# Kernel optimization log

Hardware: AMD Instinct MI355X
Metric: run time of the kernel (lower is better)

Reference implementation:

```python
import jax, jax.numpy as jnp
import numpy as np

UNITS = 64
NUM_LEVELS = 4
ORDER = 4  # order=-1 defaults to num_levels
NUM_FEATURES = 64  # 63 input features + 1 time channel
LEN_TENSORS = NUM_LEVELS * (NUM_LEVELS + 1) // 2  # 10


def setup_inputs() -> dict:
    key = jax.random.key(0)
    k1, k2 = jax.random.split(key)
    X = jax.random.normal(k1, (32, 2048, 63), dtype=jnp.float32)
    # learned low-rank kernel [num_features, len_tensors, units]; small scale keeps
    # higher-level signature products numerically tame
    kernel = jax.random.normal(k2, (NUM_FEATURES, LEN_TENSORS, UNITS), dtype=jnp.float32) * 0.02
    return {"X": X, "kernel": kernel}


def _ecumsum(x):
    # exclusive cumulative sum along time axis (axis=1), forward direction
    return jnp.cumsum(x, axis=1) - x


def reference(X, kernel):
    B, T, _ = X.shape
    # add_time=True: linear time channel in [-1, 1]
    t = jnp.arange(T, dtype=X.dtype) * (2.0 / (T - 1.0)) - 1.0
    time = jnp.broadcast_to(t[None, :, None], (B, T, 1))
    Xa = jnp.concatenate([time, X], axis=-1)  # [B, T, F]
    # low-rank projection: [B, T, len_tensors, units]
    M = jnp.einsum('btf,fku->btku', Xa, kernel)
    # difference=True: forward increments, zero-padded at t=0
    M = jnp.concatenate([jnp.zeros_like(M[:, :1]), M[:, 1:] - M[:, :-1]], axis=1)

    # level 1
    out = jnp.sum(M[..., 0, :], axis=1)  # [B, units]

    k = 1
    for m in range(1, NUM_LEVELS):
        R = [M[..., k, :]]  # list of [B, T, units]
        k += 1
        for i in range(1, m + 1):
            d = min(i + 1, ORDER)
            A = sum(R)
            Mk = M[..., k, :]
            R_next = [Mk * _ecumsum(A)]
            for j in range(1, d):
                R_next.append(Mk * R[j - 1] / jnp.asarray(j + 1, dtype=X.dtype))
            k += 1
            R = R_next
        out = out + jnp.sum(sum(R), axis=1)
    return out
```

## Files before the change

kernel.cpp:

```cpp
#include <hip/hip_runtime.h>


#define TT 2048
#define NFX 63
#define KT 10
#define NU 64
#define NQS 18
#define NCC 32
#define NSEG 4

#define MAPS_BYTES (32u * NCC * NQS * NU * 4u)
#define PLANE      40960u

typedef __attribute__((ext_vector_type(16))) float f32x16v;
typedef __attribute__((ext_vector_type(8)))  short bf16x8v;


__device__ __forceinline__ unsigned short bf16_rne(float x) {
  unsigned int u = __float_as_uint(x);
  unsigned int r = (u + 0x7FFFu + ((u >> 16) & 1u)) >> 16;
  return (unsigned short)r;
}
__device__ __forceinline__ float bf16f(unsigned short h) {
  return __uint_as_float(((unsigned int)h) << 16);
}

__device__ __forceinline__ void compose_ab(const float* q1, const float* q2,
                                           float* r)
{
  r[0] = q1[0] + q2[0] + q2[1]*q1[4] + q2[2]*q1[5] + q2[3]*q1[6];
  r[1] = q1[1] + q2[1];
  r[2] = q1[2] + q2[2] + q1[7]*q2[3];
  r[3] = q1[3] + q2[3];
  r[4] = q1[4] + q2[4];
  r[5] = q1[5] + q2[5];
  r[6] = q1[6] + q2[6] + q2[7]*q1[5];
  r[7] = q1[7] + q2[7];
}

__device__ __forceinline__ void compose_c(const float* q1, const float* q2,
                                          float* r)
{
  r[0] = q1[0] + q2[0] + q2[1]*q1[4] + q2[2]*q1[5] + q2[3]*q1[6];
  r[1] = q1[1] + q2[1] + q1[7]*q2[2] + q1[9]*q2[3];
  r[2] = q1[2] + q2[2] + q1[8]*q2[3];
  r[3] = q1[3] + q2[3];
  r[4] = q1[4] + q2[4];
  r[5] = q1[5] + q2[5] + q2[7]*q1[4];
  r[6] = q1[6] + q2[6] + q2[8]*q1[5] + q2[9]*q1[4];
  r[7] = q1[7] + q2[7];
  r[8] = q1[8] + q2[8];
  r[9] = q1[9] + q2[9] + q2[8]*q1[7];
}

__global__ __launch_bounds__(256)
void lrsig_prep_kernel(const float* __restrict__ Kw,
                       unsigned short* __restrict__ kwb)
{
  int e = blockIdx.x * 256 + threadIdx.x;
  int j  = e & 7;
  int l  = (e >> 3) & 63;
  int ks = (e >> 9) & 3;
  int ub = (e >> 11) & 1;
  int nt = e >> 12;
  int f = ks * 16 + (l >> 5) * 8 + j;
  int u = ub * 32 + (l & 31);
  float x = Kw[(f * KT + nt) * NU + u];
  unsigned short hi = bf16_rne(x);
  unsigned short lo = bf16_rne(x - bf16f(hi));
  kwb[e] = hi;
  kwb[PLANE + e] = lo;
}

#define LOADB(S) do {                                                        \
  _Pragma("unroll")                                                          \
  for (int ks = 0; ks < 4; ++ks) {                                           \
    const unsigned short* bp = kwb + ((((S) * 2 + ub) * 4 + ks) * 512) + l*8;\
    bh[ks] = *(const bf16x8v*)(bp);                                          \
    bl[ks] = *(const bf16x8v*)(bp + PLANE);                                  \
  } } while (0)

#define MFMA12(ACC) do {                                                     \
  _Pragma("unroll")                                                          \
  for (int ks = 0; ks < 4; ++ks) {                                           \
    ACC = __builtin_amdgcn_mfma_f32_32x32x16_bf16(ah[ks], bh[ks], ACC, 0,0,0); \
    ACC = __builtin_amdgcn_mfma_f32_32x32x16_bf16(al[ks], bh[ks], ACC, 0,0,0); \
    ACC = __builtin_amdgcn_mfma_f32_32x32x16_bf16(ah[ks], bl[ks], ACC, 0,0,0); \
  } } while (0)

#define ZERO(ACC) do { _Pragma("unroll")                                     \
  for (int zi = 0; zi < 16; ++zi) ACC[zi] = 0.f; } while (0)

__global__ __launch_bounds__(512)
void lrsig_chunk_kernel(const float* __restrict__ X,
                        const unsigned short* __restrict__ kwb,
                        float* __restrict__ wmaps)
{
  __shared__ __align__(16) float smemf[8192];
  char* smem = (char*)smemf;
  float* rawf = smemf + 4096;

  const int b   = blockIdx.y;
  const int c   = blockIdx.x;
  const int tid = threadIdx.x;
  const int l   = tid & 63;
  const int w   = tid >> 6;
  const int cg  = w & 1;
  const int ub  = (w >> 1) & 1;
  const int rt  = w >> 2;
  const int col = l & 31;
  const int hi8 = l >> 5;
  const int t0  = c * 64;

  float sv[8];
  {
    const float* Xb = X + (size_t)b * TT * NFX;
    const int base = (t0 - 1) * NFX;
#pragma unroll
    for (int ii = 0; ii < 8; ++ii) {
      int i = tid + ii * 512;
      int off = base + i + ((c == 0 && i < NFX) ? NFX : 0);
      sv[ii] = (i < 65 * NFX) ? Xb[off] : 0.f;
    }
  }

  bf16x8v bh[4], bl[4];
  LOADB(cg ? 6 : 0);

#pragma unroll
  for (int ii = 0; ii < 8; ++ii) {
    int i = tid + ii * 512;
    if (i < 65 * NFX) rawf[i] = sv[ii];
  }
  __syncthreads();

  {
    float v0[8], v1[8];
#pragma unroll
    for (int ii = 0; ii < 8; ++ii) {
      int e = tid + ii * 512;
      if (e < 64 * NFX) { v0[ii] = rawf[e]; v1[ii] = rawf[e + NFX]; }
    }
#pragma unroll
    for (int ii = 0; ii < 8; ++ii) {
      int e = tid + ii * 512;
      if (e < 64 * NFX) {
        int r2 = e / NFX;
        int c2 = e - r2 * NFX;
        float d = v1[ii] - v0[ii];
        unsigned short h  = bf16_rne(d);
        unsigned short lo = bf16_rne(d - bf16f(h));
        int byte = r2 * 128 + ((2 * (c2 + 1)) ^ ((r2 & 7) << 4));
        *(unsigned short*)(smem + byte)        = h;
        *(unsigned short*)(smem + 8192 + byte) = lo;
      }
    }
  }
  if (tid < 64) {
    int r2 = tid;
    float d = (t0 + r2 == 0) ? 0.f : (2.0f / 2047.0f);
    unsigned short h  = bf16_rne(d);
    unsigned short lo = bf16_rne(d - bf16f(h));
    int byte = r2 * 128 + ((0) ^ ((r2 & 7) << 4));
    *(unsigned short*)(smem + byte)        = h;
    *(unsigned short*)(smem + 8192 + byte) = lo;
  }
  __syncthreads();

  const int row = rt * 32 + col;
  const int colbase = ub * 32 + col;

  bf16x8v ah[4], al[4];
#pragma unroll
  for (int ks = 0; ks < 4; ++ks) {
    const int f0 = ks * 16 + hi8 * 8;
    const int abyte = row * 128 + ((2 * f0) ^ ((row & 7) << 4));
    ah[ks] = *(const bf16x8v*)(smem + abyte);
    al[ks] = *(const bf16x8v*)(smem + 8192 + abyte);
  }

  if (cg == 0) {
    f32x16v acc[6];
    ZERO(acc[0]); ZERO(acc[1]); ZERO(acc[2]);
    ZERO(acc[3]); ZERO(acc[4]); ZERO(acc[5]);
    MFMA12(acc[0]); LOADB(1);
    MFMA12(acc[1]); LOADB(2);
    MFMA12(acc[2]); LOADB(3);
    MFMA12(acc[3]); LOADB(4);
    MFMA12(acc[4]); LOADB(5);
    MFMA12(acc[5]);

    float tot[8];
#pragma unroll
    for (int j = 0; j < 4; ++j) {
      float oA = 0.f, a1 = 0.f, lc1 = 0.f;
      float oB = 0.f, a3 = 0.f, aA = 0.f, lc3 = 0.f, lcA = 0.f, g4 = 0.f;
#pragma unroll
      for (int i = 0; i < 4; ++i) {
        const int r = 4 * j + i;
        float m0 = acc[0][r], m1 = acc[1][r], m2 = acc[2][r];
        float m3 = acc[3][r], m4 = acc[4][r], m5 = acc[5][r];
        oA  += m0 + m2 * (lc1 + 0.5f * m1);
        a1  += m2;
        lc1 += m1;
        float s0 = m4 * lc3;
        float s1 = 0.5f * m4 * m3;
        oB  += m5 * (lcA + 0.5f * s0 + (1.f/3.f) * s1);
        a3  += m5 * (g4 + 0.5f * m4);
        aA  += m5;
        lcA += s0 + s1;
        g4  += m4;
        lc3 += m3;
      }
      float pm[8] = {oA + oB, a1, a3, aA, lc1, lc3, lcA, g4};
      float q1v[8], q2v[8], m8r[8];
#pragma unroll
      for (int q = 0; q < 8; ++q) {
        float oth = __shfl_xor(pm[q], 32);
        q1v[q] = hi8 ? oth : pm[q];
        q2v[q] = hi8 ? pm[q] : oth;
      }
      compose_ab(q1v, q2v, m8r);
      if (j == 0) {
#pragma unroll
        for (int q = 0; q < 8; ++q) tot[q] = m8r[q];
      } else {
        float nx[8];
        compose_ab(tot, m8r, nx);
#pragma unroll
        for (int q = 0; q < 8; ++q) tot[q] = nx[q];
      }
    }
    if (hi8 == 0) {
      float* p = &rawf[(rt * NQS) * NU + colbase];
#pragma unroll
      for (int q = 0; q < 8; ++q) p[q * NU] = tot[q];
    }
  } else {
    f32x16v acc[4];
    ZERO(acc[0]); ZERO(acc[1]); ZERO(acc[2]); ZERO(acc[3]);
    MFMA12(acc[0]); LOADB(7);
    MFMA12(acc[1]); LOADB(8);
    MFMA12(acc[2]); LOADB(9);
    MFMA12(acc[3]);

    float tot[10];
#pragma unroll
    for (int j = 0; j < 4; ++j) {
      float o = 0.f, a6 = 0.f, aP = 0.f, aQ = 0.f;
      float lc6 = 0.f, lcP = 0.f, lcQ = 0.f, g7 = 0.f, g8 = 0.f, hh = 0.f;
#pragma unroll
      for (int i = 0; i < 4; ++i) {
        const int r = 4 * j + i;
        float m6 = acc[0][r], m7 = acc[1][r], m8 = acc[2][r], m9 = acc[3][r];
        float p0 = m7 * lc6;
        float p1 = 0.5f * m7 * m6;
        float q0 = m8 * lcP;
        float q1 = 0.5f * m8 * p0;
        float q2 = (1.f/3.f) * m8 * p1;
        o   += m9 * (lcQ + 0.5f * q0 + (1.f/3.f) * q1 + 0.25f * q2);
        a6  += m9 * (hh + m8 * (0.5f * g7 + (1.f/6.f) * m7));
        aP  += m9 * (g8 + 0.5f * m8);
        aQ  += m9;
        hh  += m8 * (g7 + 0.5f * m7);
        lcP += p0 + p1;
        lcQ += q0 + q1 + q2;
        g7 += m7; g8 += m8; lc6 += m6;
      }
      float pm[10] = {o, a6, aP, aQ, lc6, lcP, lcQ, g7, g8, hh};
      float q1v[10], q2v[10], m8r[10];
#pragma unroll
      for (int q = 0; q < 10; ++q) {
        float oth = __shfl_xor(pm[q], 32);
        q1v[q] = hi8 ? oth : pm[q];
        q2v[q] = hi8 ? pm[q] : oth;
      }
      compose_c(q1v, q2v, m8r);
      if (j == 0) {
#pragma unroll
        for (int q = 0; q < 10; ++q) tot[q] = m8r[q];
      } else {
        float nx[10];
        compose_c(tot, m8r, nx);
#pragma unroll
        for (int q = 0; q < 10; ++q) tot[q] = nx[q];
      }
    }
    if (hi8 == 0) {
      float* p = &rawf[(rt * NQS + 8) * NU + colbase];
#pragma unroll
      for (int q = 0; q < 10; ++q) p[q * NU] = tot[q];
    }
  }
  __syncthreads();

  if (tid < NU) {
    const int uu = tid;
    float q1v[8], q2v[8], rv[8];
#pragma unroll
    for (int q = 0; q < 8; ++q) {
      q1v[q] = rawf[(0 * NQS + q) * NU + uu];
      q2v[q] = rawf[(1 * NQS + q) * NU + uu];
    }
    compose_ab(q1v, q2v, rv);
    float* p = &wmaps[(((size_t)b * NCC + c) * NQS) * NU + uu];
#pragma unroll
    for (int q = 0; q < 8; ++q) p[q * NU] = rv[q];
  } else if (tid < 2 * NU) {
    const int uu = tid - NU;
    float q1v[10], q2v[10], rv[10];
#pragma unroll
    for (int q = 0; q < 10; ++q) {
      q1v[q] = rawf[(0 * NQS + 8 + q) * NU + uu];
      q2v[q] = rawf[(1 * NQS + 8 + q) * NU + uu];
    }
    compose_c(q1v, q2v, rv);
    float* p = &wmaps[(((size_t)b * NCC + c) * NQS + 8) * NU + uu];
#pragma unroll
    for (int q = 0; q < 10; ++q) p[q * NU] = rv[q];
  }
}

__global__ __launch_bounds__(256)
void lrsig_combine_kernel(const float* __restrict__ wmaps,
                          float* __restrict__ out)
{
  __shared__ float sm[NSEG * NQS * NU];
  const int b   = blockIdx.x;
  const int seg = threadIdx.x >> 6;
  const int u   = threadIdx.x & 63;

  float tab[8], tc[10];
  {
    const float* p0 = &wmaps[(((size_t)b * NCC + seg * 8) * NQS) * NU + u];
#pragma unroll
    for (int q = 0; q < 8; ++q)  tab[q] = p0[q * NU];
#pragma unroll
    for (int q = 0; q < 10; ++q) tc[q]  = p0[(8 + q) * NU];
  }
  for (int i = 1; i < 8; ++i) {
    const float* p = &wmaps[(((size_t)b * NCC + seg * 8 + i) * NQS) * NU + u];
    float mab[8], mc[10], rab[8], rc[10];
#pragma unroll
    for (int q = 0; q < 8; ++q)  mab[q] = p[q * NU];
#pragma unroll
    for (int q = 0; q < 10; ++q) mc[q]  = p[(8 + q) * NU];
    compose_ab(tab, mab, rab);
    compose_c(tc, mc, rc);
#pragma unroll
    for (int q = 0; q < 8; ++q)  tab[q] = rab[q];
#pragma unroll
    for (int q = 0; q < 10; ++q) tc[q]  = rc[q];
  }
#pragma unroll
  for (int q = 0; q < 8; ++q)  sm[(seg * NQS + q) * NU + u]     = tab[q];
#pragma unroll
  for (int q = 0; q < 10; ++q) sm[(seg * NQS + 8 + q) * NU + u] = tc[q];
  __syncthreads();

  if (threadIdx.x < NU) {
    const int uu = threadIdx.x;
    float c1 = 0.f, c3 = 0.f, cA = 0.f, c6 = 0.f, cP = 0.f, cQ = 0.f, o = 0.f;
#pragma unroll
    for (int s = 0; s < NSEG; ++s) {
      float q[NQS];
#pragma unroll
      for (int i = 0; i < NQS; ++i) q[i] = sm[(s * NQS + i) * NU + uu];
      o  += q[0] + q[8] + q[1]*c1 + q[2]*c3 + q[3]*cA
          + q[9]*c6 + q[10]*cP + q[11]*cQ;
      cA += q[7]*c3 + q[6];
      cQ += q[16]*cP + q[17]*c6 + q[14];
      cP += q[15]*c6 + q[13];
      c1 += q[4]; c3 += q[5]; c6 += q[12];
    }
    out[b * 64 + uu] = o;
  }
}

extern "C" void kernel_launch(void* const* d_in, const int* in_sizes, int n_in,
                              void* d_out, int out_size, void* d_ws, size_t ws_size,
                              hipStream_t stream) {
  const float* X  = (const float*)d_in[0];
  const float* Kw = (const float*)d_in[1];
  float* out = (float*)d_out;
  float* wmaps = (float*)d_ws;
  unsigned short* kwb = (unsigned short*)((char*)d_ws + MAPS_BYTES);

  hipLaunchKernelGGL(lrsig_prep_kernel, dim3(160), dim3(256), 0, stream,
                     Kw, kwb);
  hipLaunchKernelGGL(lrsig_chunk_kernel, dim3(NCC, 32), dim3(512), 0, stream,
                     X, kwb, wmaps);
  hipLaunchKernelGGL(lrsig_combine_kernel, dim3(32), dim3(256), 0, stream,
                     wmaps, out);
}
```

Measured before the change: 42.10 us.

## Halve chunk length to 32 timesteps and move intra-block compose into combine

```diff
diff --git a/kernel.cpp b/kernel.cpp
--- a/kernel.cpp
+++ b/kernel.cpp
@@ -6,8 +6,8 @@
 #define KT 10
 #define NU 64
 #define NQS 18
-#define NCC 32
-#define NSEG 4
+#define NCC 64
+#define NSEG 8
 
 #define MAPS_BYTES (32u * NCC * NQS * NU * 4u)
 #define PLANE      40960u
@@ -91,14 +91,14 @@
 #define ZERO(ACC) do { _Pragma("unroll")                                     \
   for (int zi = 0; zi < 16; ++zi) ACC[zi] = 0.f; } while (0)
 
-__global__ __launch_bounds__(512)
+__global__ __launch_bounds__(256)
 void lrsig_chunk_kernel(const float* __restrict__ X,
                         const unsigned short* __restrict__ kwb,
                         float* __restrict__ wmaps)
 {
-  __shared__ __align__(16) float smemf[8192];
+  __shared__ __align__(16) float smemf[4160];
   char* smem = (char*)smemf;
-  float* rawf = smemf + 4096;
+  float* rawf = smemf + 2048;
 
   const int b   = blockIdx.y;
   const int c   = blockIdx.x;
@@ -106,21 +106,20 @@
   const int l   = tid & 63;
   const int w   = tid >> 6;
   const int cg  = w & 1;
-  const int ub  = (w >> 1) & 1;
-  const int rt  = w >> 2;
+  const int ub  = w >> 1;
   const int col = l & 31;
   const int hi8 = l >> 5;
-  const int t0  = c * 64;
-
-  float sv[8];
+  const int t0  = c * 32;
+
+  float sv[9];
   {
     const float* Xb = X + (size_t)b * TT * NFX;
     const int base = (t0 - 1) * NFX;
 #pragma unroll
-    for (int ii = 0; ii < 8; ++ii) {
-      int i = tid + ii * 512;
+    for (int ii = 0; ii < 9; ++ii) {
+      int i = tid + ii * 256;
       int off = base + i + ((c == 0 && i < NFX) ? NFX : 0);
-      sv[ii] = (i < 65 * NFX) ? Xb[off] : 0.f;
+      sv[ii] = (i < 33 * NFX) ? Xb[off] : 0.f;
     }
   }
 
@@ -128,9 +127,9 @@
   LOADB(cg ? 6 : 0);
 
 #pragma unroll
-  for (int ii = 0; ii < 8; ++ii) {
-    int i = tid + ii * 512;
-    if (i < 65 * NFX) rawf[i] = sv[ii];
+  for (int ii = 0; ii < 9; ++ii) {
+    int i = tid + ii * 256;
+    if (i < 33 * NFX) rawf[i] = sv[ii];
   }
   __syncthreads();
 
@@ -138,13 +137,13 @@
     float v0[8], v1[8];
 #pragma unroll
     for (int ii = 0; ii < 8; ++ii) {
-      int e = tid + ii * 512;
-      if (e < 64 * NFX) { v0[ii] = rawf[e]; v1[ii] = rawf[e + NFX]; }
+      int e = tid + ii * 256;
+      if (e < 32 * NFX) { v0[ii] = rawf[e]; v1[ii] = rawf[e + NFX]; }
     }
 #pragma unroll
     for (int ii = 0; ii < 8; ++ii) {
-      int e = tid + ii * 512;
-      if (e < 64 * NFX) {
+      int e = tid + ii * 256;
+      if (e < 32 * NFX) {
         int r2 = e / NFX;
         int c2 = e - r2 * NFX;
         float d = v1[ii] - v0[ii];
@@ -152,32 +151,31 @@
         unsigned short lo = bf16_rne(d - bf16f(h));
         int byte = r2 * 128 + ((2 * (c2 + 1)) ^ ((r2 & 7) << 4));
         *(unsigned short*)(smem + byte)        = h;
-        *(unsigned short*)(smem + 8192 + byte) = lo;
-      }
-    }
-  }
-  if (tid < 64) {
+        *(unsigned short*)(smem + 4096 + byte) = lo;
+      }
+    }
+  }
+  if (tid < 32) {
     int r2 = tid;
     float d = (t0 + r2 == 0) ? 0.f : (2.0f / 2047.0f);
     unsigned short h  = bf16_rne(d);
     unsigned short lo = bf16_rne(d - bf16f(h));
     int byte = r2 * 128 + ((0) ^ ((r2 & 7) << 4));
     *(unsigned short*)(smem + byte)        = h;
-    *(unsigned short*)(smem + 8192 + byte) = lo;
+    *(unsigned short*)(smem + 4096 + byte) = lo;
   }
   __syncthreads();
-
-  const int row = rt * 32 + col;
-  const int colbase = ub * 32 + col;
 
   bf16x8v ah[4], al[4];
 #pragma unroll
   for (int ks = 0; ks < 4; ++ks) {
     const int f0 = ks * 16 + hi8 * 8;
-    const int abyte = row * 128 + ((2 * f0) ^ ((row & 7) << 4));
+    const int abyte = col * 128 + ((2 * f0) ^ ((col & 7) << 4));
     ah[ks] = *(const bf16x8v*)(smem + abyte);
-    al[ks] = *(const bf16x8v*)(smem + 8192 + abyte);
-  }
+    al[ks] = *(const bf16x8v*)(smem + 4096 + abyte);
+  }
+
+  float* const mapbase = &wmaps[(((size_t)b * NCC + c) * NQS) * NU + ub * 32 + col];
 
   if (cg == 0) {
     f32x16v acc[6];
@@ -232,9 +230,8 @@
       }
     }
     if (hi8 == 0) {
-      float* p = &rawf[(rt * NQS) * NU + colbase];
-#pragma unroll
-      for (int q = 0; q < 8; ++q) p[q * NU] = tot[q];
+#pragma unroll
+      for (int q = 0; q < 8; ++q) mapbase[q * NU] = tot[q];
     }
   } else {
     f32x16v acc[4];
@@ -287,41 +284,13 @@
       }
     }
     if (hi8 == 0) {
-      float* p = &rawf[(rt * NQS + 8) * NU + colbase];
-#pragma unroll
-      for (int q = 0; q < 10; ++q) p[q * NU] = tot[q];
-    }
-  }
-  __syncthreads();
-
-  if (tid < NU) {
-    const int uu = tid;
-    float q1v[8], q2v[8], rv[8];
-#pragma unroll
-    for (int q = 0; q < 8; ++q) {
-      q1v[q] = rawf[(0 * NQS + q) * NU + uu];
-      q2v[q] = rawf[(1 * NQS + q) * NU + uu];
-    }
-    compose_ab(q1v, q2v, rv);
-    float* p = &wmaps[(((size_t)b * NCC + c) * NQS) * NU + uu];
-#pragma unroll
-    for (int q = 0; q < 8; ++q) p[q * NU] = rv[q];
-  } else if (tid < 2 * NU) {
-    const int uu = tid - NU;
-    float q1v[10], q2v[10], rv[10];
-#pragma unroll
-    for (int q = 0; q < 10; ++q) {
-      q1v[q] = rawf[(0 * NQS + 8 + q) * NU + uu];
-      q2v[q] = rawf[(1 * NQS + 8 + q) * NU + uu];
-    }
-    compose_c(q1v, q2v, rv);
-    float* p = &wmaps[(((size_t)b * NCC + c) * NQS + 8) * NU + uu];
-#pragma unroll
-    for (int q = 0; q < 10; ++q) p[q * NU] = rv[q];
-  }
-}
-
-__global__ __launch_bounds__(256)
+#pragma unroll
+      for (int q = 0; q < 10; ++q) mapbase[(8 + q) * NU] = tot[q];
+    }
+  }
+}
+
+__global__ __launch_bounds__(512)
 void lrsig_combine_kernel(const float* __restrict__ wmaps,
                           float* __restrict__ out)
 {
@@ -388,8 +357,8 @@
 
   hipLaunchKernelGGL(lrsig_prep_kernel, dim3(160), dim3(256), 0, stream,
                      Kw, kwb);
-  hipLaunchKernelGGL(lrsig_chunk_kernel, dim3(NCC, 32), dim3(512), 0, stream,
+  hipLaunchKernelGGL(lrsig_chunk_kernel, dim3(NCC, 32), dim3(256), 0, stream,
                      X, kwb, wmaps);
-  hipLaunchKernelGGL(lrsig_combine_kernel, dim3(32), dim3(256), 0, stream,
+  hipLaunchKernelGGL(lrsig_combine_kernel, dim3(32), dim3(512), 0, stream,
                      wmaps, out);
 }
```

After: 43.45 us. 1.03x slower.
